# Kernel tuning notes

Hardware: AMD Instinct MI355X
Metric: run time of the kernel (lower is better)

## Reference

```python
import jax, jax.numpy as jnp
import numpy as np

MODEL_DIM = 1024
NUM_HEADS = 16
HEAD_DIM = MODEL_DIM // NUM_HEADS
ROPE_BASE = 10000.0


def apply_rope_full(x):
    # RoPE applied over the FULL model_dim (before head split), interleaved pairs.
    B, S, D = x.shape
    half = D // 2
    inv_freq = 1.0 / (ROPE_BASE ** (jnp.arange(half, dtype=x.dtype) / half))  # [half]
    ang = jnp.arange(S, dtype=x.dtype)[:, None] * inv_freq[None, :]           # [S, half]
    cos, sin = jnp.cos(ang), jnp.sin(ang)
    x1 = x[..., 0::2]  # [B,S,half]
    x2 = x[..., 1::2]
    r1 = x1 * cos - x2 * sin
    r2 = x1 * sin + x2 * cos
    # re-interleave
    return jnp.stack([r1, r2], axis=-1).reshape(B, S, D)


def setup_inputs() -> dict:
    key = jax.random.key(0)
    ks = jax.random.split(key, 9)
    B, S, D = 4, 2048, MODEL_DIM
    sc = 1.0 / np.sqrt(D)
    inp = {
        "X": jax.random.normal(ks[0], (B, S, D), dtype=jnp.float32),
        "Wq": jax.random.normal(ks[1], (D, D), dtype=jnp.float32) * sc,
        "bq": jnp.zeros((D,), dtype=jnp.float32),
        "Wk": jax.random.normal(ks[2], (D, D), dtype=jnp.float32) * sc,
        "bk": jnp.zeros((D,), dtype=jnp.float32),
        "Wv": jax.random.normal(ks[3], (D, D), dtype=jnp.float32) * sc,
        "bv": jnp.zeros((D,), dtype=jnp.float32),
        "Wo": jax.random.normal(ks[4], (D, D), dtype=jnp.float32) * sc,
        "bo": jnp.zeros((D,), dtype=jnp.float32),
    }
    return inp


def reference(X, Wq, bq, Wk, bk, Wv, bv, Wo, bo):
    B, S, D = X.shape
    H, hd = NUM_HEADS, HEAD_DIM
    q = apply_rope_full(X @ Wq + bq)  # [B,S,D], RoPE on full dim as in source
    k = apply_rope_full(X @ Wk + bk)
    v = X @ Wv + bv
    # split heads (contiguous slices d1:d2 == reshape to [B,S,H,hd])
    qh = q.reshape(B, S, H, hd)
    kh = k.reshape(B, S, H, hd)
    vh = v.reshape(B, S, H, hd)
    scale = 1.0 / jnp.sqrt(jnp.asarray(hd, dtype=X.dtype))
    scores = jnp.einsum("bqhd,bkhd->bhqk", qh, kh) * scale  # [B,H,S,S]
    causal = jnp.tril(jnp.ones((S, S), dtype=bool))
    scores = jnp.where(causal[None, None], scores, -jnp.inf)
    weights = jax.nn.softmax(scores, axis=-1)
    attn = jnp.einsum("bhqk,bkhd->bqhd", weights, vh).reshape(B, S, D)
    return attn @ Wo + bo
```

## Files before the change

kernel.cpp:

```cpp
#include <hip/hip_runtime.h>

typedef unsigned short u16;
typedef unsigned int   u32;
typedef __attribute__((ext_vector_type(4))) float f32x4;
typedef __attribute__((ext_vector_type(8))) short short8;

#define MODEL_DIM 1024
#define SEQ 2048
#define BATCH 4
#define NHEAD 16
#define HDIM 64
#define MTOT (BATCH*SEQ)
#define ELEMS ((size_t)MTOT*MODEL_DIM)

__device__ __forceinline__ u16 f2bf(float f) {
    u32 u = __float_as_uint(f);
    u = (u + 0x7fffu + ((u >> 16) & 1u)) >> 16;
    return (u16)u;
}
__device__ __forceinline__ u32 pack2(float a, float b) {
    return (u32)f2bf(a) | ((u32)f2bf(b) << 16);
}
__device__ __forceinline__ u32 cvtpk(float lo, float hi) {
    u32 r;
    asm("v_cvt_pk_bf16_f32 %0, %1, %2" : "=v"(r) : "v"(lo), "v"(hi));
    return r;
}
__device__ __forceinline__ float exp2a(float x) {
    float r;
    asm("v_exp_f32 %0, %1" : "=v"(r) : "v"(x));
    return r;
}

#define GLOAD16(g, l) __builtin_amdgcn_global_load_lds(                        \
        (const __attribute__((address_space(1))) unsigned int*)(g),            \
        (__attribute__((address_space(3))) unsigned int*)(l), 16, 0, 0)

__global__ __launch_bounds__(256) void prep_k(const float* __restrict__ X,
                                              u16* __restrict__ Xb,
                                              const float* __restrict__ Wq,
                                              const float* __restrict__ Wk,
                                              const float* __restrict__ Wv,
                                              const float* __restrict__ Wo,
                                              u16* __restrict__ Wt) {
    const int bid = blockIdx.x, t = threadIdx.x;
    if (bid < 8192) {
        size_t i = ((size_t)bid * 256 + t) * 4;
        float4 v = *(const float4*)(X + i);
        uint2 o; o.x = pack2(v.x, v.y); o.y = pack2(v.z, v.w);
        *(uint2*)(Xb + i) = o;
        return;
    }
    __shared__ float tile[32][33];
    const int bid2 = bid - 8192;
    const int z = bid2 >> 10, rem = bid2 & 1023;
    const int by = rem >> 5, bx = rem & 31;
    const float* W = (z == 0) ? Wq : (z == 1) ? Wk : (z == 2) ? Wv : Wo;
    const int k0 = by * 32, n0 = bx * 32;
    const int x = t & 31, y = t >> 5;
    for (int i = 0; i < 4; ++i)
        tile[y + i * 8][x] = W[(size_t)(k0 + y + i * 8) * MODEL_DIM + n0 + x];
    __syncthreads();
    u16* out = Wt + ((size_t)z << 20);
    for (int i = 0; i < 4; ++i)
        out[(size_t)(n0 + y + i * 8) * MODEL_DIM + k0 + x] = f2bf(tile[x][y + i * 8]);
}

__global__ __launch_bounds__(512, 2) void gemm256qkv_k(
        const u16* __restrict__ A, const u16* __restrict__ Wt,
        u16* __restrict__ Qb, u16* __restrict__ Kb, u32* __restrict__ VT,
        const float* __restrict__ bq, const float* __restrict__ bk,
        const float* __restrict__ bv) {
    __shared__ __align__(16) u16 Ls[65536];
    const int tid  = threadIdx.x;
    const int wv   = tid >> 6, lane = tid & 63;
    const int l15  = lane & 15, quad = lane >> 4;
    const int wr = wv >> 2, wc = wv & 3;
    const int bh = wc >> 1;
    const int sb = wr * 2 + (wc & 1);
    const int m0 = blockIdx.x * 256;
    const int region = blockIdx.y >> 2;
    const int n0loc = (blockIdx.y & 3) * 256;

    const u16* Ag = A + (size_t)m0 * MODEL_DIM;
    const u16* Bg = Wt + ((size_t)region << 20) + (size_t)n0loc * MODEL_DIM;

    f32x4 acc[8][4] = {};

#define STAGE2(kt, d, q) do {                                                  \
    const int kk0_ = (kt) * 64;                                                \
    { int L_ = ((q) * 256 + wc * 64 + lane) * 16;                              \
      int P_ = L_ ^ (((L_ >> 7) & 7) << 4);                                    \
      GLOAD16(Ag + (size_t)(wr * 128 + (P_ >> 7)) * MODEL_DIM + kk0_           \
                 + ((P_ & 127) >> 1),                                          \
              &Ls[(d) * 32768 + wr * 8192 + (L_ >> 1)]); }                     \
    { int L_ = ((q) * 256 + sb * 64 + lane) * 16;                              \
      int P_ = L_ ^ (((L_ >> 7) & 7) << 4);                                    \
      GLOAD16(Bg + (size_t)(bh * 128 + (P_ >> 7)) * MODEL_DIM + kk0_           \
                 + ((P_ & 127) >> 1),                                          \
              &Ls[(d) * 32768 + 16384 + bh * 8192 + (L_ >> 1)]); }             \
} while (0)

#define LDA8(mf, ks) ({                                                        \
    int P_ = ((mf) * 16 + l15) * 128 + ((ks) * 4 + quad) * 16;                 \
    int L_ = P_ ^ (((P_ >> 7) & 7) << 4);                                      \
    *(const short8*)(ab + (L_ >> 1)); })
#define LDB8(nf, ks) ({                                                        \
    int P_ = ((wc & 1) * 64 + (nf) * 16 + l15) * 128 + ((ks) * 4 + quad) * 16; \
    int L_ = P_ ^ (((P_ >> 7) & 7) << 4);                                      \
    *(const short8*)(bb2 + (L_ >> 1)); })

#define PHASE_MFMA(MH)                                                         \
    __builtin_amdgcn_s_setprio(1);                                             \
    _Pragma("unroll")                                                          \
    for (int j2 = 0; j2 < 4; ++j2)                                             \
        _Pragma("unroll")                                                      \
        for (int nf2 = 0; nf2 < 4; ++nf2)                                      \
            acc[(MH) * 4 + j2][nf2] = __builtin_amdgcn_mfma_f32_16x16x32_bf16( \
                af[j2], bf[nf2], acc[(MH) * 4 + j2][nf2], 0, 0, 0);            \
    __builtin_amdgcn_s_setprio(0);

    STAGE2(0, 0, 0); STAGE2(0, 0, 1); STAGE2(0, 0, 2); STAGE2(0, 0, 3);

    for (int t = 0; t < 16; ++t) {
        const int pp2 = t & 1;
        const u16* ab  = &Ls[pp2 * 32768 + wr * 8192];
        const u16* bb2 = &Ls[pp2 * 32768 + 16384 + bh * 8192];
        const int dn = pp2 ^ 1;
        const bool more = (t + 1) < 16;
        short8 af[4], bf[4];
        if (more) STAGE2(t + 1, dn, 0);
        if (more) asm volatile("s_waitcnt vmcnt(2)" ::: "memory");
        else      asm volatile("s_waitcnt vmcnt(0)" ::: "memory");
        __builtin_amdgcn_s_barrier();
        __builtin_amdgcn_sched_barrier(0);
        #pragma unroll
        for (int nf = 0; nf < 4; ++nf) bf[nf] = LDB8(nf, 0);
        #pragma unroll
        for (int j = 0; j < 4; ++j) af[j] = LDA8(j, 0);
        PHASE_MFMA(0)
        __builtin_amdgcn_s_barrier();
        #pragma unroll
        for (int j = 0; j < 4; ++j) af[j] = LDA8(4 + j, 0);
        if (more) STAGE2(t + 1, dn, 1);
        __builtin_amdgcn_s_barrier();
        __builtin_amdgcn_sched_barrier(0);
        PHASE_MFMA(1)
        __builtin_amdgcn_s_barrier();
        #pragma unroll
        for (int nf = 0; nf < 4; ++nf) bf[nf] = LDB8(nf, 1);
        #pragma unroll
        for (int j = 0; j < 4; ++j) af[j] = LDA8(j, 1);
        if (more) STAGE2(t + 1, dn, 2);
        __builtin_amdgcn_s_barrier();
        __builtin_amdgcn_sched_barrier(0);
        PHASE_MFMA(0)
        __builtin_amdgcn_s_barrier();
        #pragma unroll
        for (int j = 0; j < 4; ++j) af[j] = LDA8(4 + j, 1);
        if (more) STAGE2(t + 1, dn, 3);
        __builtin_amdgcn_s_barrier();
        __builtin_amdgcn_sched_barrier(0);
        PHASE_MFMA(1)
        __builtin_amdgcn_s_barrier();
    }

    if (region < 2) {
        const float* bias = region ? bk : bq;
        u16* dst = region ? Kb : Qb;
        const float qsc = region ? 1.0f : 0.125f * 1.44269504f;
        const float cfr = -0.017989922f;
        float invf[4];
        #pragma unroll
        for (int nf = 0; nf < 4; ++nf) {
            int c = n0loc + wc * 64 + nf * 16 + l15;
            invf[nf] = __expf((float)(c >> 1) * cfr);
        }
        const float sgn = (l15 & 1) ? 1.0f : -1.0f;
        #pragma unroll
        for (int mf = 0; mf < 8; ++mf)
            #pragma unroll
            for (int r = 0; r < 4; ++r) {
                size_t rowg = (size_t)(m0 + wr * 128 + mf * 16 + quad * 4 + r);
                float fs = (float)(int)(rowg & 2047);
                #pragma unroll
                for (int nf = 0; nf < 4; ++nf) {
                    int c = n0loc + wc * 64 + nf * 16 + l15;
                    float v = acc[mf][nf][r] + bias[c];
                    float mate = __shfl_xor(v, 1, 64);
                    float sn, cs;
                    __sincosf(fs * invf[nf], &sn, &cs);
                    float o = (v * cs + sgn * mate * sn) * qsc;
                    dst[rowg * MODEL_DIM + c] = f2bf(o);
                }
            }
    } else {
        const int b_ = m0 >> 11;
        const int s0 = m0 & 2047;
        #pragma unroll
        for (int nf = 0; nf < 4; ++nf) {
            int c = n0loc + wc * 64 + nf * 16 + l15;
            float bvc = bv[c];
            u32* vtrow = VT + (size_t)((b_ * NHEAD + (c >> 6)) * HDIM
                                       + (c & 63)) * (SEQ / 2);
            #pragma unroll
            for (int mf = 0; mf < 8; ++mf) {
                int sb2 = s0 + wr * 128 + mf * 16 + quad * 4;
                uint2 w;
                w.x = cvtpk(acc[mf][nf][0] + bvc, acc[mf][nf][1] + bvc);
                w.y = cvtpk(acc[mf][nf][2] + bvc, acc[mf][nf][3] + bvc);
                *(uint2*)(vtrow + (sb2 >> 1)) = w;
            }
        }
    }
#undef STAGE2
#undef LDA8
#undef LDB8
#undef PHASE_MFMA
}

__global__ __launch_bounds__(256) void gemm128o_k(
        const u16* __restrict__ A, const u16* __restrict__ Wt,
        float* __restrict__ outO, const float* __restrict__ bo) {
    __shared__ __align__(16) u16 As[128 * 32];
    __shared__ __align__(16) u16 Bs[128 * 32];
    const int tid  = threadIdx.x;
    const int wave = tid >> 6, lane = tid & 63;
    const int l15  = lane & 15, quad = lane >> 4;
    const int wm = (wave & 1) * 64, wn = (wave >> 1) * 64;
    const int m0 = blockIdx.x * 128;
    const int n0 = blockIdx.y * 128;

    const u16* bbase = Wt + ((size_t)3 << 20) + (size_t)n0 * MODEL_DIM;
    const u16* abase = A + (size_t)m0 * MODEL_DIM;

    f32x4 acc[4][4] = {};
    const int r0 = tid >> 2, kc0 = (tid & 3) * 8;
    const u16* ga = abase + (size_t)r0 * MODEL_DIM + kc0;
    const u16* gb = bbase + (size_t)r0 * MODEL_DIM + kc0;
    u16* la0 = &As[tid * 8];
    u16* la1 = &As[2048 + tid * 8];
    u16* lb0 = &Bs[tid * 8];
    u16* lb1 = &Bs[2048 + tid * 8];

    for (int k0 = 0; k0 < MODEL_DIM; k0 += 32) {
        GLOAD16(ga + k0, la0);
        GLOAD16(ga + (size_t)64 * MODEL_DIM + k0, la1);
        GLOAD16(gb + k0, lb0);
        GLOAD16(gb + (size_t)64 * MODEL_DIM + k0, lb1);
        __syncthreads();
        short8 af[4], bf[4];
        for (int i = 0; i < 4; ++i)
            af[i] = *(const short8*)(&As[(wm + i * 16 + l15) * 32 + quad * 8]);
        for (int i = 0; i < 4; ++i)
            bf[i] = *(const short8*)(&Bs[(wn + i * 16 + l15) * 32 + quad * 8]);
        for (int mi = 0; mi < 4; ++mi)
            for (int ni = 0; ni < 4; ++ni)
                acc[mi][ni] = __builtin_amdgcn_mfma_f32_16x16x32_bf16(
                                  af[mi], bf[ni], acc[mi][ni], 0, 0, 0);
        __syncthreads();
    }

    for (int mi = 0; mi < 4; ++mi)
        for (int r = 0; r < 4; ++r) {
            size_t rowg = (size_t)(m0 + wm + mi * 16 + quad * 4 + r);
            for (int ni = 0; ni < 4; ++ni) {
                int colg = n0 + wn + ni * 16 + l15;
                outO[rowg * MODEL_DIM + colg] = acc[mi][ni][r] + bo[colg];
            }
        }
}

__global__ __launch_bounds__(256, 2) void attn_k(const u16* __restrict__ Qb,
                                                 const u16* __restrict__ Kb,
                                                 const u32* __restrict__ VT32,
                                                 u16* __restrict__ Ob) {
    __shared__ __align__(16) u16 Ks[2][64 * 64];
    __shared__ __align__(16) u16 Vs[2][64 * 64];
    __shared__ __align__(16) u16 Pl[4 * 32 * 72];
    const int tid  = threadIdx.x;
    const int wave = tid >> 6, lane = tid & 63;
    const int l15  = lane & 15, quad = lane >> 4;
    const int j = blockIdx.x;
    const int h = blockIdx.y, b = blockIdx.z;
    u16* pw = &Pl[wave * 32 * 72];

    const int key0 = tid >> 3;
    const int c8   = (tid & 7) * 8;
    const int c4   = (tid & 7) * 4;
    const int lko  = key0 * 64 + (((tid & 7) ^ (key0 & 7)) * 8);
    const u16* kgp = Kb + (size_t)(b * SEQ) * MODEL_DIM + h * HDIM;
    const u32* vgp = VT32 + (size_t)((b * NHEAD + h) * HDIM) * (SEQ / 2);

    int bufc = 0;
    for (int pp = 0; pp < 2; ++pp) {
        const int qt = pp ? j : 15 - j;
        const int q0 = qt * 128;
        const int qbase = q0 + wave * 32;

        short8 qfr[2][2];
        for (int qf = 0; qf < 2; ++qf)
            for (int ks = 0; ks < 2; ++ks)
                qfr[qf][ks] = *(const short8*)(Qb
                    + (size_t)(b * SEQ + qbase + qf * 16 + l15) * MODEL_DIM
                    + h * HDIM + ks * 32 + quad * 8);

        float m_i[2] = {-1e30f, -1e30f}, l_i[2] = {0.f, 0.f};
        f32x4 o_acc[4][2] = {};

        const int nkt = (q0 + 128) >> 6;
        uint4 kr0 = *(const uint4*)(kgp + (size_t)key0 * MODEL_DIM + c8);
        uint4 kr1 = *(const uint4*)(kgp + (size_t)(key0 + 32) * MODEL_DIM + c8);
        uint4 vr0 = *(const uint4*)(vgp + (size_t)key0 * (SEQ / 2) + c4);
        uint4 vr1 = *(const uint4*)(vgp + (size_t)(key0 + 32) * (SEQ / 2) + c4);

        for (int kt = 0; kt < nkt; ++kt) {
            const int k0 = kt * 64;
            u16* ksb = Ks[bufc];
            u16* vsb = Vs[bufc];
            *(uint4*)(&ksb[lko])        = kr0;
            *(uint4*)(&ksb[lko + 2048]) = kr1;
            *(uint4*)(&vsb[lko])        = vr0;
            *(uint4*)(&vsb[lko + 2048]) = vr1;
            __syncthreads();

            if (kt + 1 < nkt) {
                const int kn = k0 + 64;
                kr0 = *(const uint4*)(kgp + (size_t)(kn + key0) * MODEL_DIM + c8);
                kr1 = *(const uint4*)(kgp + (size_t)(kn + key0 + 32) * MODEL_DIM + c8);
                vr0 = *(const uint4*)(vgp + (size_t)key0 * (SEQ / 2) + (kn >> 1) + c4);
                vr1 = *(const uint4*)(vgp + (size_t)(key0 + 32) * (SEQ / 2)
                                      + (kn >> 1) + c4);
            }

            if (k0 <= qbase + 31) {
                f32x4 s[4][2] = {};
                for (int ks = 0; ks < 2; ++ks) {
                    short8 kfr[4];
                    for (int kf = 0; kf < 4; ++kf)
                        kfr[kf] = *(const short8*)(&ksb[(kf * 16 + l15) * 64
                                      + (((ks * 4 + quad) ^ (l15 & 7)) * 8)]);
                    __builtin_amdgcn_s_setprio(1);
                    for (int kf = 0; kf < 4; ++kf)
                        for (int qf = 0; qf < 2; ++qf)
                            s[kf][qf] = __builtin_amdgcn_mfma_f32_16x16x32_bf16(
                                            kfr[kf], qfr[qf][ks], s[kf][qf], 0, 0, 0);
                    __builtin_amdgcn_s_setprio(0);
                }
                for (int qf = 0; qf < 2; ++qf) {
                    int qg = qbase + qf * 16 + l15;
                    if (k0 + 63 > qbase + qf * 16) {
                        for (int kf = 0; kf < 4; ++kf)
                            for (int r = 0; r < 4; ++r)
                                if (k0 + kf * 16 + quad * 4 + r > qg)
                                    s[kf][qf][r] = -1e30f;
                    }
                    float t0 = fmaxf(fmaxf(s[0][qf][0], s[0][qf][1]),
                                     fmaxf(s[0][qf][2], s[0][qf][3]));
                    float t1 = fmaxf(fmaxf(s[1][qf][0], s[1][qf][1]),
                                     fmaxf(s[1][qf][2], s[1][qf][3]));
                    float t2 = fmaxf(fmaxf(s[2][qf][0], s[2][qf][1]),
                                     fmaxf(s[2][qf][2], s[2][qf][3]));
                    float t3 = fmaxf(fmaxf(s[3][qf][0], s[3][qf][1]),
                                     fmaxf(s[3][qf][2], s[3][qf][3]));
                    float rmax = fmaxf(fmaxf(t0, t1), fmaxf(t2, t3));
                    rmax = fmaxf(rmax, __shfl_xor(rmax, 16, 64));
                    rmax = fmaxf(rmax, __shfl_xor(rmax, 32, 64));
                    if (!__all(rmax <= m_i[qf] + 8.0f)) {
                        float mn = fmaxf(m_i[qf], rmax);
                        float alpha = exp2a(m_i[qf] - mn);
                        m_i[qf] = mn;
                        l_i[qf] *= alpha;
                        for (int dt = 0; dt < 4; ++dt)
                            for (int r = 0; r < 4; ++r) o_acc[dt][qf][r] *= alpha;
                    }
                    float mref = m_i[qf];
                    float psum = 0.f;
                    for (int kf = 0; kf < 4; ++kf)
                        for (int r = 0; r < 4; ++r) {
                            float p = exp2a(s[kf][qf][r] - mref);
                            s[kf][qf][r] = p;
                            psum += p;
                        }
                    psum += __shfl_xor(psum, 16, 64);
                    psum += __shfl_xor(psum, 32, 64);
                    l_i[qf] += psum;
                    for (int kf = 0; kf < 4; ++kf) {
                        uint2 w;
                        w.x = cvtpk(s[kf][qf][0], s[kf][qf][1]);
                        w.y = cvtpk(s[kf][qf][2], s[kf][qf][3]);
                        *(uint2*)(&pw[(qf * 16 + l15) * 72 + kf * 16 + quad * 4]) = w;
                    }
                }
                for (int ks = 0; ks < 2; ++ks) {
                    short8 pfr[2], vfr[4];
                    for (int qf = 0; qf < 2; ++qf)
                        pfr[qf] = *(const short8*)(&pw[(qf * 16 + l15) * 72
                                                       + ks * 32 + quad * 8]);
                    for (int dt = 0; dt < 4; ++dt)
                        vfr[dt] = *(const short8*)(&vsb[(dt * 16 + l15) * 64
                                      + (((ks * 4 + quad) ^ (l15 & 7)) * 8)]);
                    __builtin_amdgcn_s_setprio(1);
                    for (int dt = 0; dt < 4; ++dt)
                        for (int qf = 0; qf < 2; ++qf)
                            o_acc[dt][qf] = __builtin_amdgcn_mfma_f32_16x16x32_bf16(
                                                vfr[dt], pfr[qf], o_acc[dt][qf], 0, 0, 0);
                    __builtin_amdgcn_s_setprio(0);
                }
            }
            bufc ^= 1;
        }

        for (int qf = 0; qf < 2; ++qf) {
            float rl = 1.f / l_i[qf];
            int q = qbase + qf * 16 + l15;
            for (int dt = 0; dt < 4; ++dt) {
                uint2 w;
                w.x = cvtpk(o_acc[dt][qf][0] * rl, o_acc[dt][qf][1] * rl);
                w.y = cvtpk(o_acc[dt][qf][2] * rl, o_acc[dt][qf][3] * rl);
                *(uint2*)(&Ob[(size_t)(b * SEQ + q) * MODEL_DIM
                              + h * HDIM + dt * 16 + quad * 4]) = w;
            }
        }
    }
}

extern "C" void kernel_launch(void* const* d_in, const int* in_sizes, int n_in,
                              void* d_out, int out_size, void* d_ws, size_t ws_size,
                              hipStream_t stream) {
    const float* X  = (const float*)d_in[0];
    const float* Wq = (const float*)d_in[1];
    const float* bq = (const float*)d_in[2];
    const float* Wk = (const float*)d_in[3];
    const float* bk = (const float*)d_in[4];
    const float* Wv = (const float*)d_in[5];
    const float* bv = (const float*)d_in[6];
    const float* Wo = (const float*)d_in[7];
    const float* bo = (const float*)d_in[8];
    float* out = (float*)d_out;

    char* ws = (char*)d_ws;
    u16* Xb   = (u16*)ws;
    u16* Ob   = (u16*)ws;
    u16* Wt   = (u16*)(ws + 16777216);
    u16* Qb   = (u16*)(ws + 25165824);
    u16* Kb   = (u16*)(ws + 41943040);
    u32* VT32 = (u32*)(ws + 75497472);

    prep_k<<<dim3(12288), dim3(256), 0, stream>>>(X, Xb, Wq, Wk, Wv, Wo, Wt);
    gemm256qkv_k<<<dim3(32, 12), dim3(512), 0, stream>>>(Xb, Wt, Qb, Kb, VT32,
                                                         bq, bk, bv);
    attn_k<<<dim3(8, 16, 4), dim3(256), 0, stream>>>(Qb, Kb, VT32, Ob);
    gemm128o_k<<<dim3(64, 8), dim3(256), 0, stream>>>(Ob, Wt, out, bo);
}
```

Measured before the change: 264.2 us.

## Rewrite output projection GEMM as double-buffered 256x128 tile with swizzled LDS

Replaces the simple 128x128 output-projection GEMM, which synchronised twice per 32-wide k-step, with a 512-thread 256x128 tile kernel. It mirrors the QKV GEMM: a 64-wide k-step, double-buffered LDS with async global-to-LDS loads interleaved between MFMA phases, XOR-swizzled LDS addressing to avoid bank conflicts, and raised wave priority around the MFMAs. The aim is to hide load latency and raise MFMA utilisation. In exchange it launches only 256 blocks, which may underfill the GPU, and it uses much more LDS.

After: 258.3 us. 1.02x faster.

```diff
diff --git a/kernel.cpp b/kernel.cpp
--- a/kernel.cpp
+++ b/kernel.cpp
@@ -219,56 +219,120 @@
 #undef PHASE_MFMA
 }
 
-__global__ __launch_bounds__(256) void gemm128o_k(
+__global__ __launch_bounds__(512) void gemm256o_k(
         const u16* __restrict__ A, const u16* __restrict__ Wt,
         float* __restrict__ outO, const float* __restrict__ bo) {
-    __shared__ __align__(16) u16 As[128 * 32];
-    __shared__ __align__(16) u16 Bs[128 * 32];
+    __shared__ __align__(16) u16 Ls[49152];
     const int tid  = threadIdx.x;
-    const int wave = tid >> 6, lane = tid & 63;
+    const int wv   = tid >> 6, lane = tid & 63;
     const int l15  = lane & 15, quad = lane >> 4;
-    const int wm = (wave & 1) * 64, wn = (wave >> 1) * 64;
-    const int m0 = blockIdx.x * 128;
+    const int wr = wv >> 2, wc = wv & 3;
+    const int m0 = blockIdx.x * 256;
     const int n0 = blockIdx.y * 128;
 
-    const u16* bbase = Wt + ((size_t)3 << 20) + (size_t)n0 * MODEL_DIM;
-    const u16* abase = A + (size_t)m0 * MODEL_DIM;
-
-    f32x4 acc[4][4] = {};
-    const int r0 = tid >> 2, kc0 = (tid & 3) * 8;
-    const u16* ga = abase + (size_t)r0 * MODEL_DIM + kc0;
-    const u16* gb = bbase + (size_t)r0 * MODEL_DIM + kc0;
-    u16* la0 = &As[tid * 8];
-    u16* la1 = &As[2048 + tid * 8];
-    u16* lb0 = &Bs[tid * 8];
-    u16* lb1 = &Bs[2048 + tid * 8];
-
-    for (int k0 = 0; k0 < MODEL_DIM; k0 += 32) {
-        GLOAD16(ga + k0, la0);
-        GLOAD16(ga + (size_t)64 * MODEL_DIM + k0, la1);
-        GLOAD16(gb + k0, lb0);
-        GLOAD16(gb + (size_t)64 * MODEL_DIM + k0, lb1);
-        __syncthreads();
-        short8 af[4], bf[4];
-        for (int i = 0; i < 4; ++i)
-            af[i] = *(const short8*)(&As[(wm + i * 16 + l15) * 32 + quad * 8]);
-        for (int i = 0; i < 4; ++i)
-            bf[i] = *(const short8*)(&Bs[(wn + i * 16 + l15) * 32 + quad * 8]);
-        for (int mi = 0; mi < 4; ++mi)
-            for (int ni = 0; ni < 4; ++ni)
-                acc[mi][ni] = __builtin_amdgcn_mfma_f32_16x16x32_bf16(
-                                  af[mi], bf[ni], acc[mi][ni], 0, 0, 0);
-        __syncthreads();
+    const u16* Ag = A + (size_t)m0 * MODEL_DIM;
+    const u16* Bg = Wt + ((size_t)3 << 20) + (size_t)n0 * MODEL_DIM;
+
+    f32x4 acc[8][2] = {};
+
+#define STAGE_A(kt, d, q) do {                                                 \
+    const int kk0_ = (kt) * 64;                                                \
+    int L_ = ((q) * 256 + wc * 64 + lane) * 16;                                \
+    int P_ = L_ ^ (((L_ >> 7) & 7) << 4);                                      \
+    GLOAD16(Ag + (size_t)(wr * 128 + (P_ >> 7)) * MODEL_DIM + kk0_             \
+               + ((P_ & 127) >> 1),                                            \
+            &Ls[(d) * 24576 + wr * 8192 + (L_ >> 1)]);                         \
+} while (0)
+#define STAGE_B(kt, d, q) do {                                                 \
+    const int kk0_ = (kt) * 64;                                                \
+    int L_ = ((q) * 512 + tid) * 16;                                           \
+    int P_ = L_ ^ (((L_ >> 7) & 7) << 4);                                      \
+    GLOAD16(Bg + (size_t)(P_ >> 7) * MODEL_DIM + kk0_ + ((P_ & 127) >> 1),     \
+            &Ls[(d) * 24576 + 16384 + (L_ >> 1)]);                             \
+} while (0)
+
+#define LDA8O(mf, ks) ({                                                       \
+    int P_ = ((mf) * 16 + l15) * 128 + ((ks) * 4 + quad) * 16;                 \
+    int L_ = P_ ^ (((P_ >> 7) & 7) << 4);                                      \
+    *(const short8*)(ab + (L_ >> 1)); })
+#define LDB8O(nf, ks) ({                                                       \
+    int P_ = (wc * 32 + (nf) * 16 + l15) * 128 + ((ks) * 4 + quad) * 16;       \
+    int L_ = P_ ^ (((P_ >> 7) & 7) << 4);                                      \
+    *(const short8*)(bbO + (L_ >> 1)); })
+
+#define PHASE_MFMA_O(MH)                                                       \
+    __builtin_amdgcn_s_setprio(1);                                             \
+    _Pragma("unroll")                                                          \
+    for (int j2 = 0; j2 < 4; ++j2)                                             \
+        _Pragma("unroll")                                                      \
+        for (int nf2 = 0; nf2 < 2; ++nf2)                                      \
+            acc[(MH) * 4 + j2][nf2] = __builtin_amdgcn_mfma_f32_16x16x32_bf16( \
+                af[j2], bf[nf2], acc[(MH) * 4 + j2][nf2], 0, 0, 0);            \
+    __builtin_amdgcn_s_setprio(0);
+
+    STAGE_A(0, 0, 0); STAGE_B(0, 0, 0);
+    STAGE_A(0, 0, 1); STAGE_B(0, 0, 1);
+    STAGE_A(0, 0, 2); STAGE_A(0, 0, 3);
+
+    for (int t = 0; t < 16; ++t) {
+        const int pp2 = t & 1;
+        const u16* ab  = &Ls[pp2 * 24576 + wr * 8192];
+        const u16* bbO = &Ls[pp2 * 24576 + 16384];
+        const int dn = pp2 ^ 1;
+        const bool more = (t + 1) < 16;
+        short8 af[4], bf[2];
+        if (more) { STAGE_A(t + 1, dn, 0); STAGE_B(t + 1, dn, 0); }
+        if (more) asm volatile("s_waitcnt vmcnt(2)" ::: "memory");
+        else      asm volatile("s_waitcnt vmcnt(0)" ::: "memory");
+        __builtin_amdgcn_s_barrier();
+        __builtin_amdgcn_sched_barrier(0);
+        #pragma unroll
+        for (int nf = 0; nf < 2; ++nf) bf[nf] = LDB8O(nf, 0);
+        #pragma unroll
+        for (int j = 0; j < 4; ++j) af[j] = LDA8O(j, 0);
+        PHASE_MFMA_O(0)
+        __builtin_amdgcn_s_barrier();
+        #pragma unroll
+        for (int j = 0; j < 4; ++j) af[j] = LDA8O(4 + j, 0);
+        if (more) { STAGE_A(t + 1, dn, 1); STAGE_B(t + 1, dn, 1); }
+        __builtin_amdgcn_s_barrier();
+        __builtin_amdgcn_sched_barrier(0);
+        PHASE_MFMA_O(1)
+        __builtin_amdgcn_s_barrier();
+        #pragma unroll
+        for (int nf = 0; nf < 2; ++nf) bf[nf] = LDB8O(nf, 1);
+        #pragma unroll
+        for (int j = 0; j < 4; ++j) af[j] = LDA8O(j, 1);
+        if (more) STAGE_A(t + 1, dn, 2);
+        __builtin_amdgcn_s_barrier();
+        __builtin_amdgcn_sched_barrier(0);
+        PHASE_MFMA_O(0)
+        __builtin_amdgcn_s_barrier();
+        #pragma unroll
+        for (int j = 0; j < 4; ++j) af[j] = LDA8O(4 + j, 1);
+        if (more) STAGE_A(t + 1, dn, 3);
+        __builtin_amdgcn_s_barrier();
+        __builtin_amdgcn_sched_barrier(0);
+        PHASE_MFMA_O(1)
+        __builtin_amdgcn_s_barrier();
     }
 
-    for (int mi = 0; mi < 4; ++mi)
+    #pragma unroll
+    for (int mf = 0; mf < 8; ++mf)
+        #pragma unroll
         for (int r = 0; r < 4; ++r) {
-            size_t rowg = (size_t)(m0 + wm + mi * 16 + quad * 4 + r);
-            for (int ni = 0; ni < 4; ++ni) {
-                int colg = n0 + wn + ni * 16 + l15;
-                outO[rowg * MODEL_DIM + colg] = acc[mi][ni][r] + bo[colg];
+            size_t rowg = (size_t)(m0 + wr * 128 + mf * 16 + quad * 4 + r);
+            #pragma unroll
+            for (int nf = 0; nf < 2; ++nf) {
+                int colg = n0 + wc * 32 + nf * 16 + l15;
+                outO[rowg * MODEL_DIM + colg] = acc[mf][nf][r] + bo[colg];
             }
         }
+#undef STAGE_A
+#undef STAGE_B
+#undef LDA8O
+#undef LDB8O
+#undef PHASE_MFMA_O
 }
 
 __global__ __launch_bounds__(256, 2) void attn_k(const u16* __restrict__ Qb,
@@ -451,5 +515,5 @@
     gemm256qkv_k<<<dim3(32, 12), dim3(512), 0, stream>>>(Xb, Wt, Qb, Kb, VT32,
                                                          bq, bk, bv);
     attn_k<<<dim3(8, 16, 4), dim3(256), 0, stream>>>(Qb, Kb, VT32, Ob);
-    gemm128o_k<<<dim3(64, 8), dim3(256), 0, stream>>>(Ob, Wt, out, bo);
-}
+    gemm256o_k<<<dim3(32, 8), dim3(512), 0, stream>>>(Ob, Wt, out, bo);
+}
```
